# Kernel tuning notes

Measured on AMD Instinct MI355X. Metric: run time of the kernel, lower is better.

The kernel has to match this reference:

```python
import jax, jax.numpy as jnp
import numpy as np

EMBED_DIM = 1024
NUM_HEADS = 16
HEAD_DIM = EMBED_DIM // NUM_HEADS
STD = 0.02


def setup_inputs() -> dict:
    key = jax.random.key(0)
    k1, k2, k3 = jax.random.split(key, 3)
    B, S = 2, 2048
    inputs = jax.random.normal(k1, (B, S, EMBED_DIM), dtype=jnp.float32)
    # qkv projection: Linear(E, 3E); torch Linear weight is [out, in]
    w_qkv = jax.random.normal(k2, (3 * EMBED_DIM, EMBED_DIM), dtype=jnp.float32) * STD
    b_qkv = jnp.zeros((3 * EMBED_DIM,), dtype=jnp.float32)
    w_out = jax.random.normal(k3, (EMBED_DIM, EMBED_DIM), dtype=jnp.float32) * STD
    b_out = jnp.zeros((EMBED_DIM,), dtype=jnp.float32)
    return {"inputs": inputs, "w_qkv": w_qkv, "b_qkv": b_qkv, "w_out": w_out, "b_out": b_out}


def reference(inputs, w_qkv, b_qkv, w_out, b_out):
    B, S, E = inputs.shape
    qkv = inputs @ w_qkv.T + b_qkv                      # [B,S,3E]
    q, k, v = jnp.split(qkv, 3, axis=2)                 # each [B,S,E]

    def split_heads(t):
        return t.reshape(B, S, NUM_HEADS, HEAD_DIM).transpose(0, 2, 1, 3)  # [B,H,S,D]

    q, k, v = split_heads(q), split_heads(k), split_heads(v)
    scores = jnp.einsum('bhqd,bhkd->bhqk', q, k) * (1.0 / np.sqrt(HEAD_DIM))
    causal = jnp.tril(jnp.ones((S, S), dtype=bool))     # [S,S]
    scores = jnp.where(causal[None, None, :, :], scores, -jnp.inf)
    probs = jax.nn.softmax(scores, axis=-1)             # dropout is identity in eval mode
    ctx = jnp.einsum('bhqk,bhkd->bhqd', probs, v)       # [B,H,S,D]
    ctx = ctx.transpose(0, 2, 1, 3).reshape(B, S, E)
    return ctx @ w_out.T + b_out
```

## Files before the change

kernel.cpp:

```cpp
#include <hip/hip_runtime.h>
#include <hip/hip_bf16.h>

#define BATCH 2
#define SEQ   2048
#define EMB   1024
#define NHEAD 16
#define HDIM  64
#define MTOT  (BATCH*SEQ)
#define KTOT  EMB

#define NX  (MTOT*EMB)
#define NW1 (3*EMB*EMB)
#define NW2 (EMB*EMB)

typedef short bf8 __attribute__((ext_vector_type(8)));
typedef short s4v __attribute__((ext_vector_type(4)));
typedef float f4  __attribute__((ext_vector_type(4)));
typedef unsigned int uint;

__device__ __forceinline__ short f2b(float f) {
    __hip_bfloat16 h = __float2bfloat16(f);
    return __builtin_bit_cast(short, h);
}
__device__ __forceinline__ void gl_lds16(const short* g, short* l) {
    __builtin_amdgcn_global_load_lds(
        (const __attribute__((address_space(1))) uint*)g,
        (__attribute__((address_space(3))) uint*)l, 16, 0, 0);
}

__global__ __launch_bounds__(256) void cvt_all(
    const float* __restrict__ X, const float* __restrict__ W1,
    const float* __restrict__ W2,
    short* __restrict__ xb, short* __restrict__ w1b, short* __restrict__ w2b)
{
    int i4 = (blockIdx.x * 256 + threadIdx.x) * 4;
    const float* src; short* dst; int off;
    if (i4 < NX)            { src = X;  dst = xb;  off = i4; }
    else if (i4 < NX + NW1) { src = W1; dst = w1b; off = i4 - NX; }
    else                    { src = W2; dst = w2b; off = i4 - NX - NW1; }
    float4 v = *(const float4*)&src[off];
    s4v o; o[0]=f2b(v.x); o[1]=f2b(v.y); o[2]=f2b(v.z); o[3]=f2b(v.w);
    *(s4v*)&dst[off] = o;
}

#define GEMM_PROLOG(Aptr, Bptr) \
    __shared__ __align__(16) short As[128*32]; \
    __shared__ __align__(16) short Bs[128*32]; \
    const int tid  = threadIdx.x; \
    const int lane = tid & 63; \
    const int w    = tid >> 6; \
    const int l16  = lane & 15, quad = lane >> 4; \
    const int wm   = (w >> 1) * 64, wn = (w & 1) * 64; \
    const int srow = (lane >> 2); \
    const int scol = (lane & 3) * 8; \
    f4 acc[4][4] = {}; \
    for (int k0 = 0; k0 < KTOT; k0 += 32) { \
        _Pragma("unroll") \
        for (int t = 0; t < 2; t++) { \
            int ra = blockIdx.x*128 + w*32 + t*16 + srow; \
            gl_lds16(&Aptr[(size_t)ra*KTOT + k0 + scol], &As[(w*32 + t*16)*32]); \
            int rb = blockIdx.y*128 + w*32 + t*16 + srow; \
            gl_lds16(&Bptr[(size_t)rb*KTOT + k0 + scol], &Bs[(w*32 + t*16)*32]); \
        } \
        __syncthreads(); \
        bf8 af[4], bf[4]; \
        _Pragma("unroll") \
        for (int i = 0; i < 4; i++) { \
            af[i] = *(const bf8*)&As[(wm + i*16 + l16)*32 + quad*8]; \
            bf[i] = *(const bf8*)&Bs[(wn + i*16 + l16)*32 + quad*8]; \
        } \
        _Pragma("unroll") \
        for (int mt = 0; mt < 4; mt++) \
            _Pragma("unroll") \
            for (int nt = 0; nt < 4; nt++) \
                acc[mt][nt] = __builtin_amdgcn_mfma_f32_16x16x32_bf16(af[mt], bf[nt], acc[mt][nt], 0, 0, 0); \
        __syncthreads(); \
    }

__global__ __launch_bounds__(256) void gemm_qkv(
    const short* __restrict__ Xb, const short* __restrict__ Wb,
    const float* __restrict__ bias,
    short* __restrict__ qb, short* __restrict__ kb, short* __restrict__ vtb)
{
    GEMM_PROLOG(Xb, Wb)
    #pragma unroll
    for (int mt = 0; mt < 4; mt++)
    #pragma unroll
    for (int nt = 0; nt < 4; nt++) {
        int colg = blockIdx.y*128 + wn + nt*16 + l16;
        float bv = bias[colg];
        #pragma unroll
        for (int r = 0; r < 4; r++) {
            int rowg = blockIdx.x*128 + wm + mt*16 + quad*4 + r;
            short h = f2b(acc[mt][nt][r] + bv);
            int bb = rowg >> 11, s = rowg & 2047;
            if (colg < 1024) {
                int hh = colg >> 6, d = colg & 63;
                qb[(((bb*NHEAD + hh)*SEQ + s) << 6) + d] = h;
            } else if (colg < 2048) {
                int c2 = colg - 1024, hh = c2 >> 6, d = c2 & 63;
                kb[(((bb*NHEAD + hh)*SEQ + s) << 6) + d] = h;
            } else {
                int c3 = colg - 2048, hh = c3 >> 6, d = c3 & 63;
                int ssw = (s & ~63) | (((s & 15) << 2) | ((s >> 4) & 3));
                vtb[((bb*NHEAD + hh)*HDIM + d)*SEQ + ssw] = h;
            }
        }
    }
}

__global__ __launch_bounds__(256, 2) void attn(
    const short* __restrict__ qb, const short* __restrict__ kb,
    const short* __restrict__ vtb, short* __restrict__ ctx)
{
    __shared__ __align__(16) short Ks[2*2*64*32];
    __shared__ __align__(16) short Vs[2*2*64*32];
    __shared__ __align__(16) short pl[4][32*72];
    const int tid = threadIdx.x;
    const int w = tid >> 6, lane = tid & 63;
    const int l16 = lane & 15, quad = lane >> 4;
    const int f  = blockIdx.x;
    const int bh = ((f & 7) << 2) + ((f >> 3) & 3);
    const int tq = 15 - (f >> 5);
    const int q0w = tq*128 + w*32;
    const int base = bh * (SEQ*HDIM);
    short* myp = pl[w];
    const float SC = 0.125f * 1.44269504f;

    const int lq = lane >> 2;
    const int lp4 = (lane & 3) * 8;

    bf8 qa[2][2];
    #pragma unroll
    for (int m = 0; m < 2; m++)
        #pragma unroll
        for (int kc = 0; kc < 2; kc++)
            qa[m][kc] = *(const bf8*)&qb[base + (q0w + m*16 + l16)*HDIM + kc*32 + quad*8];

    f4 o[2][4] = {};
    float lacc[2][4] = {};
    const int lastj = q0w + 31;
    const int jmax  = tq*128 + 128;

    auto dma_stage = [&](int j0, int b) {
        #pragma unroll
        for (int tt = 0; tt < 4; tt++) {
            const int t = w*4 + tt;
            const int cc = t & 1, g = (t >> 1) & 3;
            if (t < 8) {
                gl_lds16(&kb[base + (j0 + g*16 + lq)*HDIM + cc*32 + lp4],
                         &Ks[b*4096 + (cc*64 + g*16)*32]);
            } else {
                gl_lds16(&vtb[base + (g*16 + lq)*SEQ + j0 + cc*32 + lp4],
                         &Vs[b*4096 + (cc*64 + g*16)*32]);
            }
        }
    };

    dma_stage(0, 0);
    __syncthreads();
    int buf = 0;
    for (int j0 = 0; j0 < jmax; j0 += 64) {
        if (j0 + 64 < jmax) dma_stage(j0 + 64, buf ^ 1);
        if (j0 <= lastj) {
            f4 s[2][4] = {};
            #pragma unroll
            for (int kf = 0; kf < 4; kf++)
                #pragma unroll
                for (int c = 0; c < 2; c++) {
                    bf8 kfr = *(const bf8*)&Ks[buf*4096 + (c*64 + kf*16 + l16)*32 + quad*8];
                    s[0][kf] = __builtin_amdgcn_mfma_f32_16x16x32_bf16(qa[0][c], kfr, s[0][kf], 0, 0, 0);
                    s[1][kf] = __builtin_amdgcn_mfma_f32_16x16x32_bf16(qa[1][c], kfr, s[1][kf], 0, 0, 0);
                }
            const bool needmask = (j0 + 63 > q0w);
            #pragma unroll
            for (int m = 0; m < 2; m++)
                #pragma unroll
                for (int r = 0; r < 4; r++) {
                    const int qi = q0w + m*16 + quad*4 + r;
                    float e[4];
                    #pragma unroll
                    for (int kf = 0; kf < 4; kf++) {
                        e[kf] = __builtin_amdgcn_exp2f(s[m][kf][r] * SC);
                        if (needmask && (j0 + kf*16 + l16 > qi)) e[kf] = 0.0f;
                        lacc[m][r] += e[kf];
                    }
                    uint u01 = __builtin_amdgcn_perm(__builtin_bit_cast(uint, e[1]),
                                                     __builtin_bit_cast(uint, e[0]), 0x07060302u);
                    uint u23 = __builtin_amdgcn_perm(__builtin_bit_cast(uint, e[3]),
                                                     __builtin_bit_cast(uint, e[2]), 0x07060302u);
                    uint2 pk = {u01, u23};
                    *(uint2*)&myp[(m*16 + quad*4 + r)*72 + l16*4] = pk;
                }
            asm volatile("" ::: "memory");
            bf8 pa[2][2];
            #pragma unroll
            for (int m = 0; m < 2; m++)
                #pragma unroll
                for (int kc = 0; kc < 2; kc++)
                    pa[m][kc] = *(const bf8*)&myp[(m*16 + l16)*72 + kc*32 + quad*8];
            #pragma unroll
            for (int dt = 0; dt < 4; dt++)
                #pragma unroll
                for (int c = 0; c < 2; c++) {
                    bf8 vf = *(const bf8*)&Vs[buf*4096 + (c*64 + dt*16 + l16)*32 + quad*8];
                    o[0][dt] = __builtin_amdgcn_mfma_f32_16x16x32_bf16(pa[0][c], vf, o[0][dt], 0, 0, 0);
                    o[1][dt] = __builtin_amdgcn_mfma_f32_16x16x32_bf16(pa[1][c], vf, o[1][dt], 0, 0, 0);
                }
        }
        __syncthreads();
        buf ^= 1;
    }
    #pragma unroll
    for (int m = 0; m < 2; m++)
        #pragma unroll
        for (int r = 0; r < 4; r++) {
            float v = lacc[m][r];
            v += __shfl_xor(v, 1);
            v += __shfl_xor(v, 2);
            v += __shfl_xor(v, 4);
            v += __shfl_xor(v, 8);
            lacc[m][r] = v;
        }
    const int b = bh >> 4, h = bh & 15;
    #pragma unroll
    for (int m = 0; m < 2; m++)
        #pragma unroll
        for (int r = 0; r < 4; r++) {
            float inv = 1.0f / lacc[m][r];
            int qi = q0w + m*16 + quad*4 + r;
            int rowoff = (b*SEQ + qi)*EMB + h*HDIM;
            #pragma unroll
            for (int dt = 0; dt < 4; dt++)
                ctx[rowoff + dt*16 + l16] = f2b(o[m][dt][r] * inv);
        }
}

__global__ __launch_bounds__(256) void gemm_out(
    const short* __restrict__ A, const short* __restrict__ Wb,
    const float* __restrict__ bias, float* __restrict__ out)
{
    GEMM_PROLOG(A, Wb)
    #pragma unroll
    for (int mt = 0; mt < 4; mt++)
    #pragma unroll
    for (int nt = 0; nt < 4; nt++) {
        int colg = blockIdx.y*128 + wn + nt*16 + l16;
        float bv = bias[colg];
        #pragma unroll
        for (int r = 0; r < 4; r++) {
            int rowg = blockIdx.x*128 + wm + mt*16 + quad*4 + r;
            out[(size_t)rowg*EMB + colg] = acc[mt][nt][r] + bv;
        }
    }
}

extern "C" void kernel_launch(void* const* d_in, const int* in_sizes, int n_in,
                              void* d_out, int out_size, void* d_ws, size_t ws_size,
                              hipStream_t stream) {
    const float* X    = (const float*)d_in[0];
    const float* Wqkv = (const float*)d_in[1];
    const float* Bqkv = (const float*)d_in[2];
    const float* Wout = (const float*)d_in[3];
    const float* Bout = (const float*)d_in[4];
    float* out = (float*)d_out;

    short* xb    = (short*)d_ws;
    short* w1b   = xb  + NX;
    short* w2b   = w1b + NW1;
    short* qb    = w2b + NW2;
    short* kb    = qb  + NX;
    short* vtb   = kb  + NX;
    short* ctx   = vtb + NX;

    cvt_all<<<(NX+NW1+NW2)/1024, 256, 0, stream>>>(X, Wqkv, Wout, xb, w1b, w2b);
    dim3 g1(MTOT/128, 3*EMB/128);
    gemm_qkv<<<g1, 256, 0, stream>>>(xb, w1b, Bqkv, qb, kb, vtb);
    attn<<<dim3(512), 256, 0, stream>>>(qb, kb, vtb, ctx);
    dim3 g3(MTOT/128, EMB/128);
    gemm_out<<<g3, 256, 0, stream>>>(ctx, w2b, Bout, out);
}
```

Measured before the change: 192.5 us.

## Halve attention query tile, double grid, and XOR-swizzle LDS tiles

The attention kernel now handles 16 query rows per wave (64 per block) instead of 32, launches 1024 blocks, and raises launch bounds to 4 blocks per CU. The aim is more parallelism and occupancy and better causal load balance. The cost is twice as many K/V loads per query row. Separately, both GEMMs and the attention K/V/P shared-memory tiles get an XOR swizzle on the global-to-LDS write and the fragment read to cut LDS bank conflicts. The P buffer shrinks from padded rows of 72 to swizzled rows of 64.

After: 183.2 us. 1.05x faster.

```diff
diff --git a/kernel.cpp b/kernel.cpp
--- a/kernel.cpp
+++ b/kernel.cpp
@@ -27,6 +27,8 @@
         (const __attribute__((address_space(1))) uint*)g,
         (__attribute__((address_space(3))) uint*)l, 16, 0, 0);
 }
+#define SWZ_SRC(lane)      ((((lane) ^ ((lane)>>2) ^ ((lane)>>4)) & 3) * 8)
+#define SWZ_RD(quad, l16)  ((((quad) ^ (l16) ^ ((l16)>>2)) & 3) * 8)
 
 __global__ __launch_bounds__(256) void cvt_all(
     const float* __restrict__ X, const float* __restrict__ W1,
@@ -52,7 +54,7 @@
     const int l16  = lane & 15, quad = lane >> 4; \
     const int wm   = (w >> 1) * 64, wn = (w & 1) * 64; \
     const int srow = (lane >> 2); \
-    const int scol = (lane & 3) * 8; \
+    const int scol = SWZ_SRC(lane); \
     f4 acc[4][4] = {}; \
     for (int k0 = 0; k0 < KTOT; k0 += 32) { \
         _Pragma("unroll") \
@@ -66,8 +68,8 @@
         bf8 af[4], bf[4]; \
         _Pragma("unroll") \
         for (int i = 0; i < 4; i++) { \
-            af[i] = *(const bf8*)&As[(wm + i*16 + l16)*32 + quad*8]; \
-            bf[i] = *(const bf8*)&Bs[(wn + i*16 + l16)*32 + quad*8]; \
+            af[i] = *(const bf8*)&As[(wm + i*16 + l16)*32 + SWZ_RD(quad, l16)]; \
+            bf[i] = *(const bf8*)&Bs[(wn + i*16 + l16)*32 + SWZ_RD(quad, l16)]; \
         } \
         _Pragma("unroll") \
         for (int mt = 0; mt < 4; mt++) \
@@ -109,38 +111,36 @@
     }
 }
 
-__global__ __launch_bounds__(256, 2) void attn(
+__global__ __launch_bounds__(256, 4) void attn(
     const short* __restrict__ qb, const short* __restrict__ kb,
     const short* __restrict__ vtb, short* __restrict__ ctx)
 {
     __shared__ __align__(16) short Ks[2*2*64*32];
     __shared__ __align__(16) short Vs[2*2*64*32];
-    __shared__ __align__(16) short pl[4][32*72];
+    __shared__ __align__(16) short pl[4][16*64];
     const int tid = threadIdx.x;
     const int w = tid >> 6, lane = tid & 63;
     const int l16 = lane & 15, quad = lane >> 4;
     const int f  = blockIdx.x;
     const int bh = ((f & 7) << 2) + ((f >> 3) & 3);
-    const int tq = 15 - (f >> 5);
-    const int q0w = tq*128 + w*32;
+    const int tq = 31 - (f >> 5);
+    const int q0w = tq*64 + w*16;
     const int base = bh * (SEQ*HDIM);
     short* myp = pl[w];
     const float SC = 0.125f * 1.44269504f;
 
-    const int lq = lane >> 2;
-    const int lp4 = (lane & 3) * 8;
-
-    bf8 qa[2][2];
-    #pragma unroll
-    for (int m = 0; m < 2; m++)
-        #pragma unroll
-        for (int kc = 0; kc < 2; kc++)
-            qa[m][kc] = *(const bf8*)&qb[base + (q0w + m*16 + l16)*HDIM + kc*32 + quad*8];
-
-    f4 o[2][4] = {};
-    float lacc[2][4] = {};
-    const int lastj = q0w + 31;
-    const int jmax  = tq*128 + 128;
+    const int lq  = lane >> 2;
+    const int lsw = SWZ_SRC(lane);
+
+    bf8 qa[2];
+    #pragma unroll
+    for (int kc = 0; kc < 2; kc++)
+        qa[kc] = *(const bf8*)&qb[base + (q0w + l16)*HDIM + kc*32 + quad*8];
+
+    f4 o[4] = {};
+    float lacc[4] = {};
+    const int lastj = q0w + 15;
+    const int jmax  = tq*64 + 64;
 
     auto dma_stage = [&](int j0, int b) {
         #pragma unroll
@@ -148,10 +148,10 @@
             const int t = w*4 + tt;
             const int cc = t & 1, g = (t >> 1) & 3;
             if (t < 8) {
-                gl_lds16(&kb[base + (j0 + g*16 + lq)*HDIM + cc*32 + lp4],
+                gl_lds16(&kb[base + (j0 + g*16 + lq)*HDIM + cc*32 + lsw],
                          &Ks[b*4096 + (cc*64 + g*16)*32]);
             } else {
-                gl_lds16(&vtb[base + (g*16 + lq)*SEQ + j0 + cc*32 + lp4],
+                gl_lds16(&vtb[base + (g*16 + lq)*SEQ + j0 + cc*32 + lsw],
                          &Vs[b*4096 + (cc*64 + g*16)*32]);
             }
         }
@@ -163,77 +163,69 @@
     for (int j0 = 0; j0 < jmax; j0 += 64) {
         if (j0 + 64 < jmax) dma_stage(j0 + 64, buf ^ 1);
         if (j0 <= lastj) {
-            f4 s[2][4] = {};
+            f4 s[4] = {};
             #pragma unroll
             for (int kf = 0; kf < 4; kf++)
                 #pragma unroll
                 for (int c = 0; c < 2; c++) {
-                    bf8 kfr = *(const bf8*)&Ks[buf*4096 + (c*64 + kf*16 + l16)*32 + quad*8];
-                    s[0][kf] = __builtin_amdgcn_mfma_f32_16x16x32_bf16(qa[0][c], kfr, s[0][kf], 0, 0, 0);
-                    s[1][kf] = __builtin_amdgcn_mfma_f32_16x16x32_bf16(qa[1][c], kfr, s[1][kf], 0, 0, 0);
+                    bf8 kfr = *(const bf8*)&Ks[buf*4096 + (c*64 + kf*16 + l16)*32 + SWZ_RD(quad, l16)];
+                    s[kf] = __builtin_amdgcn_mfma_f32_16x16x32_bf16(qa[c], kfr, s[kf], 0, 0, 0);
                 }
             const bool needmask = (j0 + 63 > q0w);
             #pragma unroll
-            for (int m = 0; m < 2; m++)
+            for (int r = 0; r < 4; r++) {
+                const int row = quad*4 + r;
+                const int qi  = q0w + row;
+                float e[4];
                 #pragma unroll
-                for (int r = 0; r < 4; r++) {
-                    const int qi = q0w + m*16 + quad*4 + r;
-                    float e[4];
-                    #pragma unroll
-                    for (int kf = 0; kf < 4; kf++) {
-                        e[kf] = __builtin_amdgcn_exp2f(s[m][kf][r] * SC);
-                        if (needmask && (j0 + kf*16 + l16 > qi)) e[kf] = 0.0f;
-                        lacc[m][r] += e[kf];
-                    }
-                    uint u01 = __builtin_amdgcn_perm(__builtin_bit_cast(uint, e[1]),
-                                                     __builtin_bit_cast(uint, e[0]), 0x07060302u);
-                    uint u23 = __builtin_amdgcn_perm(__builtin_bit_cast(uint, e[3]),
-                                                     __builtin_bit_cast(uint, e[2]), 0x07060302u);
-                    uint2 pk = {u01, u23};
-                    *(uint2*)&myp[(m*16 + quad*4 + r)*72 + l16*4] = pk;
+                for (int kf = 0; kf < 4; kf++) {
+                    e[kf] = __builtin_amdgcn_exp2f(s[kf][r] * SC);
+                    if (needmask && (j0 + kf*16 + l16 > qi)) e[kf] = 0.0f;
+                    lacc[r] += e[kf];
                 }
+                uint u01 = __builtin_amdgcn_perm(__builtin_bit_cast(uint, e[1]),
+                                                 __builtin_bit_cast(uint, e[0]), 0x07060302u);
+                uint u23 = __builtin_amdgcn_perm(__builtin_bit_cast(uint, e[3]),
+                                                 __builtin_bit_cast(uint, e[2]), 0x07060302u);
+                uint2 pk = {u01, u23};
+                int c8 = ((l16 >> 1) ^ (row & 7));
+                *(uint2*)&myp[row*64 + c8*8 + (l16 & 1)*4] = pk;
+            }
             asm volatile("" ::: "memory");
-            bf8 pa[2][2];
-            #pragma unroll
-            for (int m = 0; m < 2; m++)
-                #pragma unroll
-                for (int kc = 0; kc < 2; kc++)
-                    pa[m][kc] = *(const bf8*)&myp[(m*16 + l16)*72 + kc*32 + quad*8];
+            bf8 pa[2];
+            #pragma unroll
+            for (int kc = 0; kc < 2; kc++)
+                pa[kc] = *(const bf8*)&myp[l16*64 + (((kc*4 + quad) ^ (l16 & 7)))*8];
             #pragma unroll
             for (int dt = 0; dt < 4; dt++)
                 #pragma unroll
                 for (int c = 0; c < 2; c++) {
-                    bf8 vf = *(const bf8*)&Vs[buf*4096 + (c*64 + dt*16 + l16)*32 + quad*8];
-                    o[0][dt] = __builtin_amdgcn_mfma_f32_16x16x32_bf16(pa[0][c], vf, o[0][dt], 0, 0, 0);
-                    o[1][dt] = __builtin_amdgcn_mfma_f32_16x16x32_bf16(pa[1][c], vf, o[1][dt], 0, 0, 0);
+                    bf8 vf = *(const bf8*)&Vs[buf*4096 + (c*64 + dt*16 + l16)*32 + SWZ_RD(quad, l16)];
+                    o[dt] = __builtin_amdgcn_mfma_f32_16x16x32_bf16(pa[c], vf, o[dt], 0, 0, 0);
                 }
         }
         __syncthreads();
         buf ^= 1;
     }
     #pragma unroll
-    for (int m = 0; m < 2; m++)
-        #pragma unroll
-        for (int r = 0; r < 4; r++) {
-            float v = lacc[m][r];
-            v += __shfl_xor(v, 1);
-            v += __shfl_xor(v, 2);
-            v += __shfl_xor(v, 4);
-            v += __shfl_xor(v, 8);
-            lacc[m][r] = v;
-        }
+    for (int r = 0; r < 4; r++) {
+        float v = lacc[r];
+        v += __shfl_xor(v, 1);
+        v += __shfl_xor(v, 2);
+        v += __shfl_xor(v, 4);
+        v += __shfl_xor(v, 8);
+        lacc[r] = v;
+    }
     const int b = bh >> 4, h = bh & 15;
     #pragma unroll
-    for (int m = 0; m < 2; m++)
-        #pragma unroll
-        for (int r = 0; r < 4; r++) {
-            float inv = 1.0f / lacc[m][r];
-            int qi = q0w + m*16 + quad*4 + r;
-            int rowoff = (b*SEQ + qi)*EMB + h*HDIM;
-            #pragma unroll
-            for (int dt = 0; dt < 4; dt++)
-                ctx[rowoff + dt*16 + l16] = f2b(o[m][dt][r] * inv);
-        }
+    for (int r = 0; r < 4; r++) {
+        float inv = 1.0f / lacc[r];
+        int qi = q0w + quad*4 + r;
+        int rowoff = (b*SEQ + qi)*EMB + h*HDIM;
+        #pragma unroll
+        for (int dt = 0; dt < 4; dt++)
+            ctx[rowoff + dt*16 + l16] = f2b(o[dt][r] * inv);
+    }
 }
 
 __global__ __launch_bounds__(256) void gemm_out(
@@ -276,7 +268,7 @@
     cvt_all<<<(NX+NW1+NW2)/1024, 256, 0, stream>>>(X, Wqkv, Wout, xb, w1b, w2b);
     dim3 g1(MTOT/128, 3*EMB/128);
     gemm_qkv<<<g1, 256, 0, stream>>>(xb, w1b, Bqkv, qb, kb, vtb);
-    attn<<<dim3(512), 256, 0, stream>>>(qb, kb, vtb, ctx);
+    attn<<<dim3(1024), 256, 0, stream>>>(qb, kb, vtb, ctx);
     dim3 g3(MTOT/128, EMB/128);
     gemm_out<<<g3, 256, 0, stream>>>(ctx, w2b, Bout, out);
 }
```
